# Performance work log

Measured on AMD Instinct MI355X. Metric: run time of the kernel, lower is better.

## Reference

```python
import jax, jax.numpy as jnp
import numpy as np

HEADS = 8  # attention_heads


def setup_inputs() -> dict:
    key = jax.random.key(0)
    ks = jax.random.split(key, 6)
    B, C, H, W = 4, 256, 48, 48
    hid = 2 * C                      # per-head hidden size
    D = HEADS * hid                  # 4096
    s = 0.02
    x = jax.random.normal(ks[0], (B, C, H, W), dtype=jnp.float32)
    Wq = jax.random.normal(ks[1], (C, D), dtype=jnp.float32) * s
    Wk = jax.random.normal(ks[2], (C, D), dtype=jnp.float32) * s
    Wv = jax.random.normal(ks[3], (C, D), dtype=jnp.float32) * s
    Wo = jax.random.normal(ks[4], (D, C), dtype=jnp.float32) * s
    bq = jnp.zeros((D,), jnp.float32)
    bk = jnp.zeros((D,), jnp.float32)
    bv = jnp.zeros((D,), jnp.float32)
    bo = jnp.zeros((C,), jnp.float32)
    return {"x": x, "Wq": Wq, "bq": bq, "Wk": Wk, "bk": bk,
            "Wv": Wv, "bv": bv, "Wo": Wo, "bo": bo}


def reference(x, Wq, bq, Wk, bk, Wv, bv, Wo, bo):
    B, C, H, W = x.shape
    N = H * W
    hid = 2 * C
    A = HEADS
    # flatten spatial positions into tokens: (B, N, C)
    t = x.reshape(B, C, N).transpose(0, 2, 1)
    # project to multi-head q/k/v: (B, A, N, hid)
    def proj(Wm, bm):
        return (t @ Wm + bm).reshape(B, N, A, hid).transpose(0, 2, 1, 3)
    q = proj(Wq, bq)
    k = proj(Wk, bk)
    v = proj(Wv, bv)
    # unscaled attention (original omits 1/sqrt(d) scale)
    scores = jnp.einsum('band,bamd->banm', q, k)        # (B, A, N, N)
    attn = jax.nn.softmax(scores, axis=-1)
    o = jnp.einsum('banm,bamd->band', attn, v)          # (B, A, N, hid)
    o = o.transpose(0, 2, 1, 3).reshape(B, N, A * hid)  # (B, N, A*hid)
    out = o @ Wo + bo                                   # (B, N, C)
    return out.transpose(0, 2, 1).reshape(B, C, H, W)
```

## Files before the change

### kernel.cpp

```cpp
#include <hip/hip_runtime.h>
#include <math.h>


typedef __bf16 bf16x8 __attribute__((ext_vector_type(8)));
typedef float f32x4 __attribute__((ext_vector_type(4)));
typedef unsigned short ushort4v __attribute__((ext_vector_type(4)));

#define MFMA16(a, b, c) __builtin_amdgcn_mfma_f32_16x16x32_bf16(a, b, c, 0, 0, 0)

#define NTOK 2304
#define CIN 256
#define DTOT 4096
#define HID 512

__device__ __forceinline__ unsigned short f2bf(float f) {
  union { float f; unsigned int u; } v;
  v.f = f;
  unsigned int r = v.u + 0x7fffu + ((v.u >> 16) & 1u);
  return (unsigned short)(r >> 16);
}
__device__ __forceinline__ float bf2f(unsigned short u) {
  union { unsigned int u; float f; } v;
  v.u = (unsigned int)u << 16;
  return v.f;
}

__device__ __forceinline__ void gload16(const void* g, void* l) {
  __builtin_amdgcn_global_load_lds(
      (const __attribute__((address_space(1))) unsigned int*)g,
      (__attribute__((address_space(3))) unsigned int*)l, 16, 0, 0);
}

__device__ __forceinline__ float rsum16(float v) {
  v += __shfl_xor(v, 1);
  v += __shfl_xor(v, 2);
  v += __shfl_xor(v, 4);
  v += __shfl_xor(v, 8);
  return v;
}

__global__ void transpose_to_bf16(const float* __restrict__ src,
                                  unsigned short* __restrict__ dst,
                                  int R, int C, size_t szs, size_t dzs) {
  __shared__ float tile[32][33];
  src += (size_t)blockIdx.z * szs;
  unsigned short* d = dst + (size_t)blockIdx.z * dzs;
  int c0 = blockIdx.x * 32, r0 = blockIdx.y * 32;
  int tx = threadIdx.x, ty0 = threadIdx.y;
#pragma unroll
  for (int i = 0; i < 4; i++) {
    int ty = ty0 + i * 8;
    tile[ty][tx] = src[(size_t)(r0 + ty) * C + c0 + tx];
  }
  __syncthreads();
#pragma unroll
  for (int i = 0; i < 4; i++) {
    int ty = ty0 + i * 8;
    d[(size_t)(c0 + ty) * R + r0 + tx] = f2bf(tile[tx][ty]);
  }
}

__global__ void conv_bf16(const float* __restrict__ s0,
                          const float* __restrict__ s1,
                          const float* __restrict__ s2,
                          unsigned short* __restrict__ d0,
                          unsigned short* __restrict__ d1,
                          unsigned short* __restrict__ d2) {
  const float* s = blockIdx.y == 0 ? s0 : (blockIdx.y == 1 ? s1 : s2);
  unsigned short* d = blockIdx.y == 0 ? d0 : (blockIdx.y == 1 ? d1 : d2);
  size_t i = ((size_t)blockIdx.x * 256 + threadIdx.x) * 4;
#pragma unroll
  for (int j = 0; j < 4; j++) d[i + j] = f2bf(s[i + j]);
}

__global__ __launch_bounds__(256, 3) void hgemm(
    const unsigned short* __restrict__ A_, const unsigned short* __restrict__ B_,
    unsigned short* __restrict__ Out_) {
  __shared__ __align__(16) char smem[36864];
  unsigned short* As = (unsigned short*)smem;
  unsigned short* Bs = As + 128 * 64;
  const int z = blockIdx.z;
  const int tid = threadIdx.x;
  const int w = tid >> 6, lane = tid & 63;
  const int wr = w >> 1, wc = w & 1;
  const int l15 = lane & 15, h = lane >> 4, l7 = lane & 7;
  const int mbase = blockIdx.x * 128, nbase = blockIdx.y * 128;
  f32x4 acc[4][4] = {};
  for (int kt = 0; kt < 8; kt++) {
#pragma unroll
    for (int is = 0; is < 4; is++) {
      int row = is * 32 + (tid >> 3);
      int cl = tid & 7;
      int gc = cl ^ (row & 7);
      gload16(A_ + (size_t)(mbase + row) * DTOT + z * 512 + kt * 64 + gc * 8,
              (char*)As + row * 128 + cl * 16);
      gload16(B_ + (size_t)(nbase + row) * DTOT + z * 512 + kt * 64 + gc * 8,
              (char*)Bs + row * 128 + cl * 16);
    }
    __syncthreads();
#pragma unroll
    for (int ks = 0; ks < 2; ks++) {
      bf16x8 a[4], b[4];
#pragma unroll
      for (int m = 0; m < 4; m++)
        a[m] = *(const bf16x8*)((char*)As + (wr * 64 + m * 16 + l15) * 128 +
                                (((ks * 4 + h) ^ l7) * 16));
#pragma unroll
      for (int n = 0; n < 4; n++)
        b[n] = *(const bf16x8*)((char*)Bs + (wc * 64 + n * 16 + l15) * 128 +
                                (((ks * 4 + h) ^ l7) * 16));
#pragma unroll
      for (int m = 0; m < 4; m++)
#pragma unroll
        for (int n = 0; n < 4; n++) acc[m][n] = MFMA16(a[m], b[n], acc[m][n]);
    }
    __syncthreads();
  }
  unsigned short* ldso = (unsigned short*)(smem + w * 9216);
#pragma unroll
  for (int m = 0; m < 4; m++)
#pragma unroll
    for (int n = 0; n < 4; n++)
#pragma unroll
      for (int r = 0; r < 4; r++)
        ldso[(m * 16 + h * 4 + r) * 72 + n * 16 + l15] = f2bf(acc[m][n][r]);
  __syncthreads();
  unsigned short* Out = Out_ + (size_t)z * 65536;
#pragma unroll
  for (int pp = 0; pp < 8; pp++) {
    int q = pp * 8 + (lane >> 3);
    int ec = (lane & 7) * 8;
    *(bf16x8*)(Out + (size_t)(mbase + wr * 64 + q) * 256 + nbase + wc * 64 +
               ec) = *(const bf16x8*)(ldso + q * 72 + ec);
  }
}

__global__ void cvec_kernel(const float* __restrict__ Wk,
                            const float* __restrict__ bq,
                            float* __restrict__ cvec) {
  int z = blockIdx.x, c = threadIdx.x;
  float s = 0.f;
  const float* wr_ = Wk + (size_t)c * DTOT + z * 512;
  const float* br = bq + z * 512;
  for (int e = 0; e < 512; e++) s += br[e] * wr_[e];
  cvec[z * 256 + c] = s;
}

__global__ void dvec_kernel(const float* __restrict__ Wo,
                            const float* __restrict__ bv,
                            float* __restrict__ dvec) {
  int z = blockIdx.x, c = threadIdx.x;
  float s = 0.f;
  const float* br = bv + z * 512;
  const float* wr_ = Wo + (size_t)z * 512 * CIN + c;
  for (int e = 0; e < 512; e++) s += br[e] * wr_[(size_t)e * CIN];
  dvec[z * 256 + c] = s;
}

__global__ __launch_bounds__(256, 3) void proj2(
    const unsigned short* __restrict__ Tb, const unsigned short* __restrict__ H,
    const float* __restrict__ cvec, const unsigned short* __restrict__ M,
    unsigned short* __restrict__ Uo, unsigned short* __restrict__ VWo) {
  __shared__ __align__(16) char smem[36864];
  unsigned short* As = (unsigned short*)smem;
  unsigned short* Bs = As + 128 * 64;
  const int bb = blockIdx.z;
  const unsigned short* T = Tb + (size_t)bb * NTOK * CIN;
  int y = blockIdx.y;
  const unsigned short* B;
  const float* bias;
  unsigned short* Out;
  int layout;
  if (y < 16) {
    B = H; bias = cvec; Out = Uo; layout = 0;
  } else {
    B = M; bias = nullptr; Out = VWo; layout = 1; y -= 16;
  }
  const int tid = threadIdx.x;
  const int w = tid >> 6, lane = tid & 63;
  const int wr = w >> 1, wc = w & 1;
  const int l15 = lane & 15, h = lane >> 4, l7 = lane & 7;
  const int mbase = blockIdx.x * 128, nglob = y * 128;
  f32x4 acc[4][4] = {};
  for (int kt = 0; kt < 4; kt++) {
#pragma unroll
    for (int is = 0; is < 4; is++) {
      int row = is * 32 + (tid >> 3);
      int cl = tid & 7;
      int gc = cl ^ (row & 7);
      gload16(T + (size_t)(mbase + row) * CIN + kt * 64 + gc * 8,
              (char*)As + row * 128 + cl * 16);
      gload16(B + (size_t)(nglob + row) * 256 + kt * 64 + gc * 8,
              (char*)Bs + row * 128 + cl * 16);
    }
    __syncthreads();
#pragma unroll
    for (int ks = 0; ks < 2; ks++) {
      bf16x8 a[4], b[4];
#pragma unroll
      for (int m = 0; m < 4; m++)
        a[m] = *(const bf16x8*)((char*)As + (wr * 64 + m * 16 + l15) * 128 +
                                (((ks * 4 + h) ^ l7) * 16));
#pragma unroll
      for (int n = 0; n < 4; n++)
        b[n] = *(const bf16x8*)((char*)Bs + (wc * 64 + n * 16 + l15) * 128 +
                                (((ks * 4 + h) ^ l7) * 16));
#pragma unroll
      for (int m = 0; m < 4; m++)
#pragma unroll
        for (int n = 0; n < 4; n++) acc[m][n] = MFMA16(a[m], b[n], acc[m][n]);
    }
    __syncthreads();
  }
  float bias_n[4];
#pragma unroll
  for (int n = 0; n < 4; n++)
    bias_n[n] = bias ? bias[nglob + wc * 64 + n * 16 + l15] : 0.f;
  unsigned short* ldso = (unsigned short*)(smem + w * 9216);
  const int ntok0 = mbase + wr * 64;
  const int z = nglob >> 8;
  const int col0 = (nglob & 255) + wc * 64;
  if (layout == 0) {
#pragma unroll
    for (int m = 0; m < 4; m++)
#pragma unroll
      for (int n = 0; n < 4; n++)
#pragma unroll
        for (int r = 0; r < 4; r++)
          ldso[(m * 16 + h * 4 + r) * 72 + n * 16 + l15] =
              f2bf(acc[m][n][r] + bias_n[n]);
    __syncthreads();
#pragma unroll
    for (int pp = 0; pp < 8; pp++) {
      int q = pp * 8 + (lane >> 3);
      int ec = (lane & 7) * 8;
      *(bf16x8*)(Out + (((size_t)bb * 8 + z) * NTOK + ntok0 + q) * 256 + col0 +
                 ec) = *(const bf16x8*)(ldso + q * 72 + ec);
    }
  } else {
#pragma unroll
    for (int m = 0; m < 4; m++)
#pragma unroll
      for (int n = 0; n < 4; n++)
#pragma unroll
        for (int r = 0; r < 4; r++)
          ldso[(n * 16 + l15) * 72 + m * 16 + h * 4 + r] =
              f2bf(acc[m][n][r] + bias_n[n]);
    __syncthreads();
#pragma unroll
    for (int pp = 0; pp < 8; pp++) {
      int cc = pp * 8 + (lane >> 3);
      int tc = (lane & 7) * 8;
      *(bf16x8*)(Out + (((size_t)bb * 8 + z) * 256 + col0 + cc) * NTOK +
                 ntok0 + tc) = *(const bf16x8*)(ldso + cc * 72 + tc);
    }
  }
}

__global__ __launch_bounds__(256, 2) void fused_attn(
    const unsigned short* __restrict__ Ub, const unsigned short* __restrict__ Tb,
    const unsigned short* __restrict__ VWoT, unsigned short* __restrict__ Opart,
    float* __restrict__ l_part) {
  __shared__ __align__(16) char smem[73728];
  unsigned short* Ts = (unsigned short*)smem;
  unsigned short* Ws = (unsigned short*)(smem + 32768);
  unsigned short* Ps = (unsigned short*)(smem + 65536);
  const int i = blockIdx.x;
  const int z = i & 7;
  const int s = (i >> 3) & 1;
  const int qt = (i >> 4) % 36;
  const int bb = (i >> 4) / 36;
  const int q0 = qt * 64;
  const int k0 = s * 1152;
  const int tid = threadIdx.x;
  const int w = tid >> 6, lane = tid & 63;
  const int l15 = lane & 15, h = lane >> 4;

  const unsigned short* U = Ub + ((size_t)bb * 8 + z) * NTOK * 256;
  const unsigned short* T = Tb + (size_t)bb * NTOK * CIN;
  const unsigned short* Wv = VWoT + ((size_t)bb * 8 + z) * 256 * NTOK;

#pragma unroll
  for (int it = 0; it < 8; it++) {
    int f = it * 256 + tid;
    int row = f >> 5, cb = f & 31;
    gload16(U + (size_t)(q0 + row) * 256 + (size_t)((cb ^ (row & 7)) * 8),
            (char*)smem + (size_t)f * 16);
  }
  __syncthreads();
  bf16x8 ua[8];
  {
    int q = w * 16 + l15;
#pragma unroll
    for (int ks = 0; ks < 8; ks++)
      ua[ks] = *(const bf16x8*)((char*)Ts + q * 512 +
                                (((ks * 4 + h) ^ (q & 7)) * 16));
  }
  f32x4 oacc[4][4] = {};
  float lacc[4] = {0.f, 0.f, 0.f, 0.f};
  __syncthreads();

  for (int kt = 0; kt < 18; kt++) {
    const int kb = k0 + kt * 64;
#pragma unroll
    for (int it = 0; it < 8; it++) {
      int f = it * 256 + tid;
      int row = f >> 5, cb = f & 31;
      gload16(T + (size_t)(kb + row) * 256 + (size_t)((cb ^ (row & 7)) * 8),
              (char*)smem + (size_t)f * 16);
    }
#pragma unroll
    for (int it = 0; it < 8; it++) {
      int row = it * 32 + (tid >> 3);
      int cl = tid & 7, gc = cl ^ (row & 7);
      gload16(Wv + (size_t)row * NTOK + kb + gc * 8,
              (char*)Ws + row * 128 + cl * 16);
    }
    __syncthreads();
    f32x4 sacc[4] = {};
    __builtin_amdgcn_s_setprio(1);
#pragma unroll
    for (int ks = 0; ks < 8; ks++) {
#pragma unroll
      for (int kf = 0; kf < 4; kf++) {
        int key = kf * 16 + l15;
        bf16x8 tb_ = *(const bf16x8*)((char*)Ts + key * 512 +
                                      (((ks * 4 + h) ^ (key & 7)) * 16));
        sacc[kf] = MFMA16(ua[ks], tb_, sacc[kf]);
      }
    }
    __builtin_amdgcn_s_setprio(0);
#pragma unroll
    for (int kf = 0; kf < 4; kf++)
#pragma unroll
      for (int r = 0; r < 4; r++) {
        float pv = __expf(sacc[kf][r]);
        lacc[r] += pv;
        int q = w * 16 + h * 4 + r;
        int k = kf * 16 + l15;
        Ps[q * 64 + (((k >> 3) ^ (q & 7)) << 3) + (k & 7)] = f2bf(pv);
      }
    __syncthreads();
    __builtin_amdgcn_s_setprio(1);
#pragma unroll
    for (int ks2 = 0; ks2 < 2; ks2++) {
      bf16x8 pa[4];
#pragma unroll
      for (int m = 0; m < 4; m++) {
        int q = m * 16 + l15;
        pa[m] = *(const bf16x8*)((char*)Ps + q * 128 +
                                 (((ks2 * 4 + h) ^ (q & 7)) * 16));
      }
#pragma unroll
      for (int n = 0; n < 4; n++) {
        int c = w * 64 + n * 16 + l15;
        bf16x8 wb = *(const bf16x8*)((char*)Ws + c * 128 +
                                     (((ks2 * 4 + h) ^ (c & 7)) * 16));
#pragma unroll
        for (int m = 0; m < 4; m++) oacc[m][n] = MFMA16(pa[m], wb, oacc[m][n]);
      }
    }
    __builtin_amdgcn_s_setprio(0);
    __syncthreads();
  }
#pragma unroll
  for (int r = 0; r < 4; r++) {
    float v = rsum16(lacc[r]);
    if (l15 == 0)
      l_part[(((size_t)bb * 2 + s) * 8 + z) * NTOK + q0 + w * 16 + h * 4 + r] =
          v;
  }
  unsigned short* ldso = (unsigned short*)(smem + w * 9216);
#pragma unroll
  for (int m = 0; m < 4; m++)
#pragma unroll
    for (int n = 0; n < 4; n++)
#pragma unroll
      for (int r = 0; r < 4; r++)
        ldso[(n * 16 + l15) * 72 + m * 16 + h * 4 + r] = f2bf(oacc[m][n][r]);
  unsigned short* Out =
      Opart + ((((size_t)bb * 2 + s) * 8 + z) * 256 + w * 64) * NTOK + q0;
#pragma unroll
  for (int pp = 0; pp < 8; pp++) {
    int cc = pp * 8 + (lane >> 3);
    int qc = (lane & 7) * 8;
    *(bf16x8*)(Out + (size_t)cc * NTOK + qc) =
        *(const bf16x8*)(ldso + cc * 72 + qc);
  }
}

__global__ void reduce_out2(const unsigned short* __restrict__ Opart,
                            const float* __restrict__ l_part,
                            const float* __restrict__ dvec,
                            const float* __restrict__ bo,
                            float* __restrict__ out) {
  const int bb = blockIdx.y;
  int idx = (blockIdx.x * 256 + threadIdx.x) * 4;
  int c = idx / NTOK;
  int q = idx - c * NTOK;
  const unsigned short* Ob = Opart + (size_t)bb * 2 * 8 * 256 * NTOK;
  const float* lb = l_part + (size_t)bb * 2 * 8 * NTOK;
  f32x4 acc = {bo[c], bo[c], bo[c], bo[c]};
#pragma unroll
  for (int z = 0; z < 8; z++) {
    ushort4v o0 = *(const ushort4v*)&Ob[((size_t)z * 256 + c) * NTOK + q];
    ushort4v o1 = *(const ushort4v*)&Ob[((size_t)(8 + z) * 256 + c) * NTOK + q];
    f32x4 l0 = *(const f32x4*)&lb[(size_t)z * NTOK + q];
    f32x4 l1 = *(const f32x4*)&lb[(size_t)(8 + z) * NTOK + q];
    float d = dvec[z * 256 + c];
#pragma unroll
    for (int j = 0; j < 4; j++)
      acc[j] += (bf2f(o0[j]) + bf2f(o1[j])) / (l0[j] + l1[j]) + d;
  }
  *(f32x4*)&out[(size_t)bb * CIN * NTOK + idx] = acc;
}

extern "C" void kernel_launch(void* const* d_in, const int* in_sizes, int n_in,
                              void* d_out, int out_size, void* d_ws,
                              size_t ws_size, hipStream_t stream) {
  const float* x = (const float*)d_in[0];
  const float* Wq = (const float*)d_in[1];
  const float* bq = (const float*)d_in[2];
  const float* Wk = (const float*)d_in[3];
  const float* bk = (const float*)d_in[4];
  const float* Wv = (const float*)d_in[5];
  const float* bv = (const float*)d_in[6];
  const float* Wo = (const float*)d_in[7];
  const float* bo = (const float*)d_in[8];
  float* out = (float*)d_out;
  (void)bk;

  unsigned short* Wq_bf = (unsigned short*)d_ws;
  unsigned short* Wk_bf = Wq_bf + 1048576;
  unsigned short* Wv_bf = Wk_bf + 1048576;
  unsigned short* WoT = Wv_bf + 1048576;
  unsigned short* Hmat = WoT + 1048576;
  unsigned short* MmatT = Hmat + 524288;
  float* cvec = (float*)(MmatT + 524288);
  float* dvec = cvec + 2048;
  unsigned short* tb = (unsigned short*)(dvec + 2048);
  unsigned short* Uc = tb + 4ull * 589824;
  unsigned short* VWoT = Uc + 32ull * 589824;
  unsigned short* Opart = VWoT + 32ull * 589824;
  float* l_part = (float*)(Opart + 64ull * 589824);
  size_t need_el = (size_t)((unsigned short*)(l_part + 4 * 2 * 8 * NTOK) -
                            (unsigned short*)d_ws);
  if (ws_size / 2 < need_el) return;

  dim3 tp(32, 8);
  conv_bf16<<<dim3(1024, 3), 256, 0, stream>>>(Wq, Wk, Wv, Wq_bf, Wk_bf,
                                               Wv_bf);
  transpose_to_bf16<<<dim3(72, 8, 4), tp, 0, stream>>>(
      x, tb, CIN, NTOK, (size_t)CIN * NTOK, (size_t)NTOK * CIN);
  transpose_to_bf16<<<dim3(8, 128, 1), tp, 0, stream>>>(Wo, WoT, DTOT, CIN, 0,
                                                        0);
  hgemm<<<dim3(2, 2, 8), 256, 0, stream>>>(Wk_bf, Wq_bf, Hmat);
  hgemm<<<dim3(2, 2, 8), 256, 0, stream>>>(WoT, Wv_bf, MmatT);
  cvec_kernel<<<dim3(8), 256, 0, stream>>>(Wk, bq, cvec);
  dvec_kernel<<<dim3(8), 256, 0, stream>>>(Wo, bv, dvec);

  proj2<<<dim3(18, 32, 4), 256, 0, stream>>>(tb, Hmat, cvec, MmatT, Uc, VWoT);
  fused_attn<<<dim3(2304), 256, 0, stream>>>(Uc, tb, VWoT, Opart, l_part);
  reduce_out2<<<dim3(576, 4), 256, 0, stream>>>(Opart, l_part, dvec, bo, out);
}
```

Measured before the change: 350.1 us.

## Double attention query tile to 128 with 512-thread blocks and pack P stores

The fused attention kernel now handles 128 queries per block with 8 waves instead of 64 queries with 4 waves. The waves split into two query halves and four output-column slices, so each loaded key tile and V·Wo tile serves twice as many queries. This halves global and LDS refill traffic per query and halves the grid size. Probabilities are now packed two bf16 per 32-bit LDS store via a lane shuffle. In exchange, LDS per block grows and the stricter launch bounds (512,4) may cap registers tightly enough to cause spills of the accumulators.

Result: slower. 748.6 us (+113.8%).

```diff
diff --git a/kernel.cpp b/kernel.cpp
--- a/kernel.cpp
+++ b/kernel.cpp
@@ -257,20 +257,20 @@
   }
 }
 
-__global__ __launch_bounds__(256, 2) void fused_attn(
+__global__ __launch_bounds__(512, 4) void fused_attn(
     const unsigned short* __restrict__ Ub, const unsigned short* __restrict__ Tb,
     const unsigned short* __restrict__ VWoT, unsigned short* __restrict__ Opart,
     float* __restrict__ l_part) {
-  __shared__ __align__(16) char smem[73728];
+  __shared__ __align__(16) char smem[81920];
   unsigned short* Ts = (unsigned short*)smem;
   unsigned short* Ws = (unsigned short*)(smem + 32768);
   unsigned short* Ps = (unsigned short*)(smem + 65536);
   const int i = blockIdx.x;
   const int z = i & 7;
   const int s = (i >> 3) & 1;
-  const int qt = (i >> 4) % 36;
-  const int bb = (i >> 4) / 36;
-  const int q0 = qt * 64;
+  const int qt = (i >> 4) % 18;
+  const int bb = (i >> 4) / 18;
+  const int q0 = qt * 128;
   const int k0 = s * 1152;
   const int tid = threadIdx.x;
   const int w = tid >> 6, lane = tid & 63;
@@ -280,39 +280,45 @@
   const unsigned short* T = Tb + (size_t)bb * NTOK * CIN;
   const unsigned short* Wv = VWoT + ((size_t)bb * 8 + z) * 256 * NTOK;
 
-#pragma unroll
-  for (int it = 0; it < 8; it++) {
-    int f = it * 256 + tid;
-    int row = f >> 5, cb = f & 31;
-    gload16(U + (size_t)(q0 + row) * 256 + (size_t)((cb ^ (row & 7)) * 8),
-            (char*)smem + (size_t)f * 16);
-  }
-  __syncthreads();
   bf16x8 ua[8];
-  {
-    int q = w * 16 + l15;
-#pragma unroll
-    for (int ks = 0; ks < 8; ks++)
-      ua[ks] = *(const bf16x8*)((char*)Ts + q * 512 +
-                                (((ks * 4 + h) ^ (q & 7)) * 16));
+#pragma unroll
+  for (int half = 0; half < 2; half++) {
+#pragma unroll
+    for (int it = 0; it < 4; it++) {
+      int f = it * 512 + tid;
+      int row = f >> 5, cb = f & 31;
+      gload16(U + (size_t)(q0 + half * 64 + row) * 256 +
+                  (size_t)((cb ^ (row & 7)) * 8),
+              (char*)smem + (size_t)f * 16);
+    }
+    __syncthreads();
+    if ((w >> 2) == half) {
+      int lrow = (w & 3) * 16 + l15;
+#pragma unroll
+      for (int ks = 0; ks < 8; ks++)
+        ua[ks] = *(const bf16x8*)((char*)Ts + lrow * 512 +
+                                  (((ks * 4 + h) ^ (lrow & 7)) * 16));
+    }
+    __syncthreads();
   }
   f32x4 oacc[4][4] = {};
   float lacc[4] = {0.f, 0.f, 0.f, 0.f};
-  __syncthreads();
+  const int qh = w >> 2, cs = w & 3;
 
   for (int kt = 0; kt < 18; kt++) {
     const int kb = k0 + kt * 64;
 #pragma unroll
-    for (int it = 0; it < 8; it++) {
-      int f = it * 256 + tid;
+    for (int it = 0; it < 4; it++) {
+      int f = it * 512 + tid;
       int row = f >> 5, cb = f & 31;
       gload16(T + (size_t)(kb + row) * 256 + (size_t)((cb ^ (row & 7)) * 8),
               (char*)smem + (size_t)f * 16);
     }
 #pragma unroll
-    for (int it = 0; it < 8; it++) {
-      int row = it * 32 + (tid >> 3);
-      int cl = tid & 7, gc = cl ^ (row & 7);
+    for (int it = 0; it < 4; it++) {
+      int f = it * 512 + tid;
+      int row = f >> 3, cl = f & 7;
+      int gc = cl ^ (row & 7);
       gload16(Wv + (size_t)row * NTOK + kb + gc * 8,
               (char*)Ws + row * 128 + cl * 16);
     }
@@ -336,9 +342,15 @@
       for (int r = 0; r < 4; r++) {
         float pv = __expf(sacc[kf][r]);
         lacc[r] += pv;
-        int q = w * 16 + h * 4 + r;
-        int k = kf * 16 + l15;
-        Ps[q * 64 + (((k >> 3) ^ (q & 7)) << 3) + (k & 7)] = f2bf(pv);
+        float pn = __shfl_xor(pv, 1);
+        if ((l15 & 1) == 0) {
+          int q = w * 16 + h * 4 + r;
+          int k = kf * 16 + l15;
+          unsigned int pk =
+              (unsigned int)f2bf(pv) | ((unsigned int)f2bf(pn) << 16);
+          *(unsigned int*)((char*)Ps + q * 128 + (((k >> 3) ^ (q & 7)) << 4) +
+                           ((k & 7) << 1)) = pk;
+        }
       }
     __syncthreads();
     __builtin_amdgcn_s_setprio(1);
@@ -347,13 +359,13 @@
       bf16x8 pa[4];
 #pragma unroll
       for (int m = 0; m < 4; m++) {
-        int q = m * 16 + l15;
+        int q = qh * 64 + m * 16 + l15;
         pa[m] = *(const bf16x8*)((char*)Ps + q * 128 +
                                  (((ks2 * 4 + h) ^ (q & 7)) * 16));
       }
 #pragma unroll
       for (int n = 0; n < 4; n++) {
-        int c = w * 64 + n * 16 + l15;
+        int c = cs * 64 + n * 16 + l15;
         bf16x8 wb = *(const bf16x8*)((char*)Ws + c * 128 +
                                      (((ks2 * 4 + h) ^ (c & 7)) * 16));
 #pragma unroll
@@ -378,8 +390,8 @@
 #pragma unroll
       for (int r = 0; r < 4; r++)
         ldso[(n * 16 + l15) * 72 + m * 16 + h * 4 + r] = f2bf(oacc[m][n][r]);
-  unsigned short* Out =
-      Opart + ((((size_t)bb * 2 + s) * 8 + z) * 256 + w * 64) * NTOK + q0;
+  unsigned short* Out = Opart +
+      ((((size_t)bb * 2 + s) * 8 + z) * 256 + cs * 64) * NTOK + q0 + qh * 64;
 #pragma unroll
   for (int pp = 0; pp < 8; pp++) {
     int cc = pp * 8 + (lane >> 3);
@@ -460,6 +472,6 @@
   dvec_kernel<<<dim3(8), 256, 0, stream>>>(Wo, bv, dvec);
 
   proj2<<<dim3(18, 32, 4), 256, 0, stream>>>(tb, Hmat, cvec, MmatT, Uc, VWoT);
-  fused_attn<<<dim3(2304), 256, 0, stream>>>(Uc, tb, VWoT, Opart, l_part);
+  fused_attn<<<dim3(1152), 512, 0, stream>>>(Uc, tb, VWoT, Opart, l_part);
   reduce_out2<<<dim3(576, 4), 256, 0, stream>>>(Opart, l_part, dvec, bo, out);
 }
```
